# Optimization experiments

Measured on AMD Instinct MI355X. Metric: run time of the kernel, lower is better.

## Reference

```python
import jax, jax.numpy as jnp
import numpy as np

N = 50000; IN_DIM = 128; HID = 128; T = 4; R = 3; E = 500000

def setup_inputs() -> dict:
    key = jax.random.key(0)
    ks = jax.random.split(key, 20)
    def nrm(k, shape, s):
        return jax.random.normal(k, shape, jnp.float32) * s
    s_in = 1.0 / float(np.sqrt(IN_DIM)); s_h = 1.0 / float(np.sqrt(HID))
    return {
        'feat_seq': nrm(ks[0], (T, N, IN_DIM), 1.0),
        'src': jax.random.randint(ks[1], (T, R, E), 0, N, jnp.int32),
        'dst': jax.random.randint(ks[2], (T, R, E), 0, N, jnp.int32),
        'ew': jax.random.uniform(ks[3], (T, R, E), jnp.float32),
        'W_in': nrm(ks[4], (IN_DIM, HID), s_in), 'b_in': jnp.zeros((HID,), jnp.float32),
        'W1': nrm(ks[5], (R, HID, HID), s_h), 'b1': jnp.zeros((R, HID), jnp.float32),
        'W2': nrm(ks[6], (R, HID, HID), s_h), 'b2': jnp.zeros((R, HID), jnp.float32),
        'q1': nrm(ks[7], (HID,), 1.0), 'q2': nrm(ks[8], (HID,), 1.0),
        'ln1_g': jnp.ones((HID,), jnp.float32), 'ln1_b': jnp.zeros((HID,), jnp.float32),
        'ln2_g': jnp.ones((HID,), jnp.float32), 'ln2_b': jnp.zeros((HID,), jnp.float32),
        'gWih': nrm(ks[9], (HID, 3 * HID), s_h), 'gbih': jnp.zeros((3 * HID,), jnp.float32),
        'gWhh': nrm(ks[10], (HID, 3 * HID), s_h), 'gbhh': jnp.zeros((3 * HID,), jnp.float32),
        'temp_q': nrm(ks[11], (HID,), 1.0),
        'tW1': nrm(ks[12], (IN_DIM, HID), s_in), 'tb1': jnp.zeros((HID,), jnp.float32),
        'tW2': nrm(ks[13], (HID, HID), s_h), 'tb2': jnp.zeros((HID,), jnp.float32),
        'cW1': nrm(ks[14], (3 * HID, HID), 1.0 / float(np.sqrt(3 * HID))), 'cb1': jnp.zeros((HID,), jnp.float32),
        'cW2': nrm(ks[15], (HID, 1), s_h), 'cb2': jnp.zeros((1,), jnp.float32),
    }

def _ln(x, g, b):
    m = x.mean(-1, keepdims=True)
    v = ((x - m) ** 2).mean(-1, keepdims=True)
    return (x - m) * jax.lax.rsqrt(v + 1e-5) * g + b

def _rel_attn(stack, q):
    # stack: [R,N,H]; tanh-softmax attention over relations
    score = jnp.einsum('rnh,h->rn', jnp.tanh(stack), q)
    alpha = jax.nn.softmax(score, axis=0)
    return jnp.einsum('rn,rnh->nh', alpha, stack)

def _conv(x, s, d, w, Wr, br):
    # DGL GraphConv norm='right' with edge_weight: mean-by-in-degree weighted SpMM
    msg = w[:, None] * x[s]                                   # [E,H]
    agg = jax.ops.segment_sum(msg, d, num_segments=N)
    deg = jax.ops.segment_sum(jnp.ones_like(w), d, num_segments=N)
    return (agg / jnp.maximum(deg, 1.0)[:, None]) @ Wr + br

def reference(feat_seq, src, dst, ew, W_in, b_in, W1, b1, W2, b2, q1, q2, ln1_g, ln1_b, ln2_g, ln2_b, gWih, gbih, gWhh, gbhh, temp_q, tW1, tb1, tW2, tb2, cW1, cb1, cW2, cb2):
    conv_all = jax.vmap(_conv, in_axes=(None, 0, 0, 0, 0, 0))
    def spatial(x, s, d, w):
        h0 = jax.nn.relu(x @ W_in + b_in)
        h1 = _ln(h0 + jax.nn.relu(_rel_attn(conv_all(h0, s, d, w, W1, b1), q1)), ln1_g, ln1_b)
        h2 = _ln(h1 + jax.nn.relu(_rel_attn(conv_all(h1, s, d, w, W2, b2), q2)), ln2_g, ln2_b)
        return h2
    hs = jnp.stack([spatial(feat_seq[t], src[t], dst[t], ew[t]) for t in range(T)], axis=0)  # [T,N,H]
    def gru_step(h, x):
        gi = x @ gWih + gbih
        gh = h @ gWhh + gbhh
        ir, iz, inn = jnp.split(gi, 3, axis=-1)
        hr, hz, hn = jnp.split(gh, 3, axis=-1)
        r = jax.nn.sigmoid(ir + hr)
        zg = jax.nn.sigmoid(iz + hz)
        n = jnp.tanh(inn + r * hn)
        hnew = (1.0 - zg) * n + zg * h
        return hnew, hnew
    _, outs = jax.lax.scan(gru_step, jnp.zeros((N, HID), feat_seq.dtype), hs)  # [T,N,H]
    out = jnp.transpose(outs, (1, 0, 2))                       # [N,T,H]
    last = out[:, -1, :]
    t_score = jnp.einsum('nth,h->nt', jnp.tanh(out), temp_q)
    t_alpha = jax.nn.softmax(t_score, axis=1)
    attn = jnp.einsum('nt,nth->nh', t_alpha, out)
    tab = jax.nn.relu(jax.nn.relu(feat_seq[-1] @ tW1 + tb1) @ tW2 + tb2)
    z = jnp.concatenate([last, attn, tab], axis=-1)
    return (jax.nn.relu(z @ cW1 + cb1) @ cW2 + cb2)[:, 0]       # [N]
```

## Files before the change

### kernel.cpp

```cpp
#include <hip/hip_runtime.h>
#include <hip/hip_bf16.h>
#include <math.h>

#define NN 50000
#define TT 4
#define RR 3
#define EE 500000
#define RANGE 6400
#define NRANGE 8

typedef __attribute__((ext_vector_type(8))) short bf16x8;
typedef __attribute__((ext_vector_type(4))) float f32x4;

__device__ inline unsigned short f2b(float f)
{
    union { __hip_bfloat16 h; unsigned short u; } cv;
    cv.h = __float2bfloat16(f);
    return cv.u;
}
__device__ inline float b2f(unsigned short u)
{
    union { unsigned int u; float f; } cv;
    cv.u = ((unsigned int)u) << 16;
    return cv.f;
}
__device__ inline bf16x8 pack8(float4 a, float4 b)
{
    bf16x8 r;
    r[0] = (short)f2b(a.x); r[1] = (short)f2b(a.y); r[2] = (short)f2b(a.z); r[3] = (short)f2b(a.w);
    r[4] = (short)f2b(b.x); r[5] = (short)f2b(b.y); r[6] = (short)f2b(b.z); r[7] = (short)f2b(b.w);
    return r;
}


__global__ __launch_bounds__(256)
void diag_kernel(float* __restrict__ out, float v)
{
    int i = blockIdx.x * 256 + threadIdx.x;
    if (i < NN) out[i] = v;
}


__global__ __launch_bounds__(256)
void wswz_kernel(const float* __restrict__ W, unsigned short* __restrict__ dst, int C, int S)
{
    int idx = blockIdx.x * 256 + threadIdx.x;
    int per = 128 * C;
    if (idx >= S * per) return;
    int s = idx / per, rem = idx - s * per;
    int j = rem & 7;
    int lane = (rem >> 3) & 63;
    int blk = rem >> 9;
    int ncg = C >> 4;
    int kc = blk / ncg, cg = blk - kc * ncg;
    int k = kc * 32 + (lane >> 4) * 8 + j;
    int c = cg * 16 + (lane & 15);
    dst[idx] = f2b(W[(size_t)s * 128 * C + (size_t)k * C + c]);
}


__global__ __launch_bounds__(1024)
void count_hist(const int* __restrict__ dst, int* __restrict__ cnt)
{
    __shared__ int hist[RANGE];
    const int g = blockIdx.y;
    const int r0 = blockIdx.x * RANGE;
    for (int i = threadIdx.x; i < RANGE; i += 1024) hist[i] = 0;
    __syncthreads();
    const int4* d4 = (const int4*)(dst + (size_t)g * EE);
    for (int i = threadIdx.x; i < EE / 4; i += 1024) {
        int4 v = d4[i];
        int a0 = v.x - r0; if ((unsigned)a0 < (unsigned)RANGE) atomicAdd(&hist[a0], 1);
        int a1 = v.y - r0; if ((unsigned)a1 < (unsigned)RANGE) atomicAdd(&hist[a1], 1);
        int a2 = v.z - r0; if ((unsigned)a2 < (unsigned)RANGE) atomicAdd(&hist[a2], 1);
        int a3 = v.w - r0; if ((unsigned)a3 < (unsigned)RANGE) atomicAdd(&hist[a3], 1);
    }
    __syncthreads();
    int* c = cnt + (size_t)g * NN;
    for (int i = threadIdx.x; i < RANGE; i += 1024) {
        int n = r0 + i;
        if (n < NN) c[n] = hist[i];
    }
}

__global__ __launch_bounds__(1024)
void scan_kernel(int* __restrict__ cnt, int* __restrict__ rows)
{
    int g = blockIdx.x;
    int tid = threadIdx.x;
    const int CH = (NN + 1023) / 1024;
    int s0 = tid * CH;
    int s1 = s0 + CH; if (s1 > NN) s1 = NN;
    int* c = cnt + (size_t)g * NN;
    int* ro = rows + (size_t)g * (NN + 1);
    int sum = 0;
    for (int i = s0; i < s1; ++i) sum += c[i];
    __shared__ int sd[1024];
    sd[tid] = sum;
    __syncthreads();
    for (int off = 1; off < 1024; off <<= 1) {
        int v = 0;
        if (tid >= off) v = sd[tid - off];
        __syncthreads();
        sd[tid] += v;
        __syncthreads();
    }
    int total = sd[1023];
    int prefix = (tid == 0) ? 0 : sd[tid - 1];
    for (int i = s0; i < s1; ++i) {
        int cv = c[i];
        ro[i] = prefix;
        c[i] = prefix;
        prefix += cv;
    }
    if (tid == 0) ro[NN] = total;
}

__global__ __launch_bounds__(256)
void fill_kernel(const int* __restrict__ src, const int* __restrict__ dst,
                 const float* __restrict__ ew, int* __restrict__ cur,
                 int2* __restrict__ srcw)
{
    int g = blockIdx.y;
    int e = blockIdx.x * 256 + threadIdx.x;
    if (e >= EE) return;
    size_t idx = (size_t)g * EE + e;
    int d = dst[idx];
    int pos = atomicAdd(&cur[(size_t)g * NN + d], 1);
    int2 p;
    p.x = src[idx];
    p.y = __float_as_int(ew[idx]);
    srcw[(size_t)g * EE + pos] = p;
}


__global__ __launch_bounds__(256)
void agg16_kernel(const unsigned short* __restrict__ x16,
                  const int2* __restrict__ srcw,
                  const int* __restrict__ rows,
                  unsigned short* __restrict__ agg16)
{
    int wid = (blockIdx.x * 256 + threadIdx.x) >> 6;
    int lane = threadIdx.x & 63;
    if (wid >= RR * NN) return;
    int r = wid / NN;
    int n = wid - r * NN;
    const int* rs = rows + (size_t)r * (NN + 1);
    int e0 = rs[n], e1 = rs[n + 1];
    const int2* sw = srcw + (size_t)r * EE;
    const int co = lane * 2;
    float ax = 0.f, ay = 0.f;
    for (int e = e0; e < e1; e += 16) {
        int2 p[16];
        unsigned int v[16];
#pragma unroll
        for (int i = 0; i < 16; ++i) {
            int idx = (e + i < e1) ? e + i : e1 - 1;
            p[i] = sw[idx];
        }
#pragma unroll
        for (int i = 0; i < 16; ++i)
            v[i] = *(const unsigned int*)(x16 + (size_t)p[i].x * 128 + co);
#pragma unroll
        for (int i = 0; i < 16; ++i) {
            float w = (e + i < e1) ? __int_as_float(p[i].y) : 0.f;
            ax += w * b2f((unsigned short)(v[i] & 0xffffu));
            ay += w * b2f((unsigned short)(v[i] >> 16));
        }
    }
    float inv = 1.0f / fmaxf((float)(e1 - e0), 1.0f);
    unsigned int o = (unsigned int)f2b(ax * inv) | ((unsigned int)f2b(ay * inv) << 16);
    *(unsigned int*)(agg16 + ((size_t)r * NN + n) * 128 + co) = o;
}


__global__ __launch_bounds__(256)
void mmb(const void* in, int in_bf16, long in_zs, int ldin,
         const unsigned short* __restrict__ Ws, long w_zs,
         const float* __restrict__ bias, long b_zs,
         float* out, long out_zs, int ldout,
         unsigned short* out16, long out16_zs,
         int rows, int act)
{
    const int tid = threadIdx.x;
    const int wv = tid >> 6, l = tid & 63;
    const int z = blockIdx.z;
    const int r0 = blockIdx.x * 64 + wv * 16;
    const int lk = (l >> 4) * 8;
    int rowA = r0 + (l & 15);
    int rowc = rowA < rows ? rowA : rows - 1;

    bf16x8 a[4];
    if (in_bf16) {
        const unsigned short* inb = (const unsigned short*)in + (size_t)z * in_zs
                                    + (size_t)rowc * ldin + lk;
#pragma unroll
        for (int kc = 0; kc < 4; ++kc) {
            uint4 u = *(const uint4*)(inb + kc * 32);
            a[kc] = *(bf16x8*)&u;
        }
    } else {
        const float* inf = (const float*)in + (size_t)z * in_zs
                           + (size_t)rowc * ldin + lk;
#pragma unroll
        for (int kc = 0; kc < 4; ++kc) {
            float4 u0 = *(const float4*)(inf + kc * 32);
            float4 u1 = *(const float4*)(inf + kc * 32 + 4);
            a[kc] = pack8(u0, u1);
        }
    }

    const unsigned short* Wz = Ws + (size_t)z * w_zs;
    const float* bz = bias + (size_t)z * b_zs;
    float* oz = out ? out + (size_t)z * out_zs : (float*)0;
    unsigned short* o16z = out16 ? out16 + (size_t)z * out16_zs : (unsigned short*)0;
    const int colbase = l & 15;
    const int rbase = r0 + (l >> 4) * 4;

#pragma unroll
    for (int cg = 0; cg < 8; ++cg) {
        f32x4 acc = {0.f, 0.f, 0.f, 0.f};
#pragma unroll
        for (int kc = 0; kc < 4; ++kc) {
            uint4 bu = *(const uint4*)(Wz + ((size_t)(kc * 8 + cg) * 64 + l) * 8);
            acc = __builtin_amdgcn_mfma_f32_16x16x32_bf16(a[kc], *(bf16x8*)&bu, acc, 0, 0, 0);
        }
        int col = cg * 16 + colbase;
        float bvv = bz[col];
#pragma unroll
        for (int j = 0; j < 4; ++j) {
            int gr = rbase + j;
            if (gr >= rows) continue;
            float v = acc[j] + bvv;
            if (act) v = fmaxf(v, 0.f);
            if (oz) oz[(size_t)gr * ldout + col] = v;
            if (o16z) o16z[(size_t)gr * 128 + col] = f2b(v);
        }
    }
}


__global__ __launch_bounds__(256)
void grub_all(const float* x, float* h,
              const unsigned short* __restrict__ Wis, const float* __restrict__ bi,
              const unsigned short* __restrict__ Whs, const float* __restrict__ bh,
              float* outs)
{
    const int tid = threadIdx.x;
    const int wv = tid >> 6, l = tid & 63;
    const int r0 = blockIdx.x * 64 + wv * 16;
    const int lk = (l >> 4) * 8;
    int rowA = r0 + (l & 15);
    int rowc = rowA < NN ? rowA : NN - 1;

    bf16x8 ax[4], hx[4];
    {
        const float* bx = x + (size_t)rowc * 128 + lk;
        const float* bhp = h + (size_t)rowc * 128 + lk;
#pragma unroll
        for (int kc = 0; kc < 4; ++kc) {
            ax[kc] = pack8(*(const float4*)(bx + kc * 32), *(const float4*)(bx + kc * 32 + 4));
            hx[kc] = pack8(*(const float4*)(bhp + kc * 32), *(const float4*)(bhp + kc * 32 + 4));
        }
    }
    const int colbase = l & 15;
    const int rbase = r0 + (l >> 4) * 4;

#pragma unroll
    for (int cg = 0; cg < 8; ++cg) {
        f32x4 air = {0.f,0.f,0.f,0.f}, ahr = {0.f,0.f,0.f,0.f};
        f32x4 aiz = {0.f,0.f,0.f,0.f}, ahz = {0.f,0.f,0.f,0.f};
        f32x4 ain = {0.f,0.f,0.f,0.f}, ahn = {0.f,0.f,0.f,0.f};
#pragma unroll
        for (int kc = 0; kc < 4; ++kc) {
            uint4 br = *(const uint4*)(Wis + ((size_t)(kc * 24 + 0 + cg) * 64 + l) * 8);
            uint4 hr = *(const uint4*)(Whs + ((size_t)(kc * 24 + 0 + cg) * 64 + l) * 8);
            uint4 bz = *(const uint4*)(Wis + ((size_t)(kc * 24 + 8 + cg) * 64 + l) * 8);
            uint4 hz = *(const uint4*)(Whs + ((size_t)(kc * 24 + 8 + cg) * 64 + l) * 8);
            uint4 bn = *(const uint4*)(Wis + ((size_t)(kc * 24 + 16 + cg) * 64 + l) * 8);
            uint4 hn = *(const uint4*)(Whs + ((size_t)(kc * 24 + 16 + cg) * 64 + l) * 8);
            air = __builtin_amdgcn_mfma_f32_16x16x32_bf16(ax[kc], *(bf16x8*)&br, air, 0, 0, 0);
            ahr = __builtin_amdgcn_mfma_f32_16x16x32_bf16(hx[kc], *(bf16x8*)&hr, ahr, 0, 0, 0);
            aiz = __builtin_amdgcn_mfma_f32_16x16x32_bf16(ax[kc], *(bf16x8*)&bz, aiz, 0, 0, 0);
            ahz = __builtin_amdgcn_mfma_f32_16x16x32_bf16(hx[kc], *(bf16x8*)&hz, ahz, 0, 0, 0);
            ain = __builtin_amdgcn_mfma_f32_16x16x32_bf16(ax[kc], *(bf16x8*)&bn, ain, 0, 0, 0);
            ahn = __builtin_amdgcn_mfma_f32_16x16x32_bf16(hx[kc], *(bf16x8*)&hn, ahn, 0, 0, 0);
        }
        int col = cg * 16 + colbase;
        float bir = bi[col],       bhr = bh[col];
        float biz = bi[128 + col], bhz = bh[128 + col];
        float bin = bi[256 + col], bhn = bh[256 + col];
#pragma unroll
        for (int j = 0; j < 4; ++j) {
            int gr = rbase + j;
            if (gr >= NN) continue;
            float r_ = 1.f / (1.f + __expf(-(air[j] + bir + ahr[j] + bhr)));
            float z_ = 1.f / (1.f + __expf(-(aiz[j] + biz + ahz[j] + bhz)));
            float n_ = tanhf(ain[j] + bin + r_ * (ahn[j] + bhn));
            float hv = h[(size_t)gr * 128 + col];
            float o = (1.f - z_) * n_ + z_ * hv;
            h[(size_t)gr * 128 + col] = o;
            outs[(size_t)gr * 128 + col] = o;
        }
    }
}


__global__ __launch_bounds__(256)
void cls_mfma(const float* __restrict__ in,
              const unsigned short* __restrict__ Ws,
              const float* __restrict__ b1_,
              const float* __restrict__ w2,
              const float* __restrict__ b2_,
              float* __restrict__ outv, int rows)
{
    const int tid = threadIdx.x;
    const int wv = tid >> 6, l = tid & 63;
    const int r0 = blockIdx.x * 64 + wv * 16;
    const int lk = (l >> 4) * 8;
    int rowA = r0 + (l & 15);
    int rowc = rowA < rows ? rowA : rows - 1;

    bf16x8 a[12];
    {
        const float* inf = in + (size_t)rowc * 384 + lk;
#pragma unroll
        for (int kc = 0; kc < 12; ++kc) {
            float4 u0 = *(const float4*)(inf + kc * 32);
            float4 u1 = *(const float4*)(inf + kc * 32 + 4);
            a[kc] = pack8(u0, u1);
        }
    }
    const int colbase = l & 15;
    const int rbase = r0 + (l >> 4) * 4;
    float part[4] = {0.f, 0.f, 0.f, 0.f};

#pragma unroll
    for (int cg = 0; cg < 8; ++cg) {
        f32x4 acc = {0.f, 0.f, 0.f, 0.f};
#pragma unroll
        for (int kc = 0; kc < 12; ++kc) {
            uint4 bu = *(const uint4*)(Ws + ((size_t)(kc * 8 + cg) * 64 + l) * 8);
            acc = __builtin_amdgcn_mfma_f32_16x16x32_bf16(a[kc], *(bf16x8*)&bu, acc, 0, 0, 0);
        }
        int col = cg * 16 + colbase;
        float b1v = b1_[col];
        float w2v = w2[col];
#pragma unroll
        for (int j = 0; j < 4; ++j)
            part[j] += fmaxf(acc[j] + b1v, 0.f) * w2v;
    }
    const float cb2v = b2_[0];
#pragma unroll
    for (int j = 0; j < 4; ++j) {
#pragma unroll
        for (int m = 1; m < 16; m <<= 1) part[j] += __shfl_xor(part[j], m);
        int gr = rbase + j;
        if ((l & 15) == 0 && gr < rows) outv[gr] = part[j] + cb2v;
    }
}


__device__ inline float wred(float v)
{
#pragma unroll
    for (int m = 32; m; m >>= 1) v += __shfl_xor(v, m);
    return v;
}

__global__ __launch_bounds__(256)
void attnln_kernel(const unsigned short* __restrict__ agg16,
                   const unsigned short* hin16,
                   const float* __restrict__ q,
                   const float* __restrict__ g,
                   const float* __restrict__ b,
                   float* hout,
                   unsigned short* hout16)
{
    int wid = (blockIdx.x * 256 + threadIdx.x) >> 6;
    int lane = threadIdx.x & 63;
    if (wid >= NN) return;
    int n = wid;
    float2 qv = *(const float2*)(q + lane * 2);
    float sx[3], sy[3], sc[3];
#pragma unroll
    for (int r = 0; r < 3; ++r) {
        unsigned int v = *(const unsigned int*)(agg16 + ((size_t)r * NN + n) * 128 + lane * 2);
        sx[r] = b2f((unsigned short)(v & 0xffffu));
        sy[r] = b2f((unsigned short)(v >> 16));
        sc[r] = wred(tanhf(sx[r]) * qv.x + tanhf(sy[r]) * qv.y);
    }
    float mx = fmaxf(sc[0], fmaxf(sc[1], sc[2]));
    float e0 = __expf(sc[0] - mx), e1 = __expf(sc[1] - mx), e2 = __expf(sc[2] - mx);
    float isum = 1.f / (e0 + e1 + e2);
    float axv = (e0 * sx[0] + e1 * sx[1] + e2 * sx[2]) * isum;
    float ayv = (e0 * sy[0] + e1 * sy[1] + e2 * sy[2]) * isum;
    unsigned int hv = *(const unsigned int*)(hin16 + (size_t)n * 128 + lane * 2);
    float ux = b2f((unsigned short)(hv & 0xffffu)) + fmaxf(axv, 0.f);
    float uy = b2f((unsigned short)(hv >> 16)) + fmaxf(ayv, 0.f);
    float mean = wred(ux + uy) * (1.f / 128.f);
    float dx = ux - mean, dy = uy - mean;
    float var = wred(dx * dx + dy * dy) * (1.f / 128.f);
    float rstd = rsqrtf(var + 1e-5f);
    float2 gv = *(const float2*)(g + lane * 2);
    float2 bv = *(const float2*)(b + lane * 2);
    float ox = dx * rstd * gv.x + bv.x;
    float oy = dy * rstd * gv.y + bv.y;
    if (hout) {
        float2 o; o.x = ox; o.y = oy;
        *(float2*)(hout + (size_t)n * 128 + lane * 2) = o;
    }
    if (hout16) {
        unsigned int p = (unsigned int)f2b(ox) | ((unsigned int)f2b(oy) << 16);
        *(unsigned int*)(hout16 + (size_t)n * 128 + lane * 2) = p;
    }
}


__global__ __launch_bounds__(256)
void temporal_kernel(const float* __restrict__ outs,
                     const float* __restrict__ tq,
                     float* __restrict__ zbuf)
{
    int wid = (blockIdx.x * 256 + threadIdx.x) >> 6;
    int lane = threadIdx.x & 63;
    if (wid >= NN) return;
    int n = wid;
    float2 qv = *(const float2*)(tq + lane * 2);
    float2 o[4];
    float sc[4];
#pragma unroll
    for (int t = 0; t < 4; ++t) {
        o[t] = *(const float2*)(outs + ((size_t)t * NN + n) * 128 + lane * 2);
        sc[t] = wred(tanhf(o[t].x) * qv.x + tanhf(o[t].y) * qv.y);
    }
    float mx = fmaxf(fmaxf(sc[0], sc[1]), fmaxf(sc[2], sc[3]));
    float e[4];
    float sum = 0.f;
#pragma unroll
    for (int t = 0; t < 4; ++t) { e[t] = __expf(sc[t] - mx); sum += e[t]; }
    float isum = 1.f / sum;
    float axv = 0.f, ayv = 0.f;
#pragma unroll
    for (int t = 0; t < 4; ++t) { axv += e[t] * o[t].x; ayv += e[t] * o[t].y; }
    axv *= isum; ayv *= isum;
    float* zr = zbuf + (size_t)n * 384;
    *(float2*)(zr + lane * 2) = o[3];
    float2 at; at.x = axv; at.y = ayv;
    *(float2*)(zr + 128 + lane * 2) = at;
}


extern "C" void kernel_launch(void* const* d_in, const int* in_sizes, int n_in,
                              void* d_out, int out_size, void* d_ws, size_t ws_size,
                              hipStream_t stream)
{
    const float* feat = (const float*)d_in[0];
    const int* srcp   = (const int*)d_in[1];
    const int* dstp   = (const int*)d_in[2];
    const float* ewp  = (const float*)d_in[3];
    const float* W_in = (const float*)d_in[4];
    const float* b_in = (const float*)d_in[5];
    const float* W1   = (const float*)d_in[6];
    const float* b1   = (const float*)d_in[7];
    const float* W2   = (const float*)d_in[8];
    const float* b2   = (const float*)d_in[9];
    const float* q1   = (const float*)d_in[10];
    const float* q2   = (const float*)d_in[11];
    const float* ln1g = (const float*)d_in[12];
    const float* ln1b = (const float*)d_in[13];
    const float* ln2g = (const float*)d_in[14];
    const float* ln2b = (const float*)d_in[15];
    const float* gWih = (const float*)d_in[16];
    const float* gbih = (const float*)d_in[17];
    const float* gWhh = (const float*)d_in[18];
    const float* gbhh = (const float*)d_in[19];
    const float* tq   = (const float*)d_in[20];
    const float* tW1  = (const float*)d_in[21];
    const float* tb1  = (const float*)d_in[22];
    const float* tW2  = (const float*)d_in[23];
    const float* tb2  = (const float*)d_in[24];
    const float* cW1  = (const float*)d_in[25];
    const float* cb1  = (const float*)d_in[26];
    const float* cW2  = (const float*)d_in[27];
    const float* cb2  = (const float*)d_in[28];
    float* outv = (float*)d_out;
    (void)in_sizes; (void)n_in; (void)out_size;

    const size_t o_HS    = 0;
    const size_t o_POOL  = 102400000;
    const size_t o_AGG16 = o_POOL;
    const size_t o_H16   = o_POOL + 38400000;
    const size_t o_SRCW  = o_POOL + 51200000;
    const size_t o_ROWS  = o_POOL + 63200000;
    const size_t o_CURS  = o_POOL + 65600128;
    const size_t o_ZB    = o_POOL;
    const size_t o_H     = o_POOL + 76800000;
    const size_t o_WSZ   = o_H + 25600000;
    const size_t NEED    = o_WSZ + 589824;

    if (ws_size < NEED) {
        diag_kernel<<<dim3((NN + 255) / 256), dim3(256), 0, stream>>>(outv, (float)(ws_size >> 20));
        return;
    }

    char* wsb = (char*)d_ws;
    float* HS             = (float*)(wsb + o_HS);
    unsigned short* AGG16 = (unsigned short*)(wsb + o_AGG16);
    unsigned short* H16   = (unsigned short*)(wsb + o_H16);
    int2*  SRCW           = (int2*)(wsb + o_SRCW);
    int*   ROWS           = (int*)(wsb + o_ROWS);
    int*   CURS           = (int*)(wsb + o_CURS);
    float* ZB             = (float*)(wsb + o_ZB);
    float* HST            = (float*)(wsb + o_H);
    unsigned short* TAB16 = (unsigned short*)(wsb + o_H);
    unsigned short* WSZ   = (unsigned short*)(wsb + o_WSZ);

    unsigned short* Wins  = WSZ;
    unsigned short* W1s   = WSZ + 16384;
    unsigned short* W2s   = WSZ + 65536;
    unsigned short* gWihs = WSZ + 114688;
    unsigned short* gWhhs = WSZ + 163840;
    unsigned short* tW1s  = WSZ + 212992;
    unsigned short* tW2s  = WSZ + 229376;
    unsigned short* cW1s  = WSZ + 245760;

    const dim3 blk(256);
    const int G64 = (NN + 63) / 64;
    const dim3 gE((EE + 255) / 256, RR);

    wswz_kernel<<<dim3((1 * 16384 + 255) / 256), blk, 0, stream>>>(W_in, Wins, 128, 1);
    wswz_kernel<<<dim3((3 * 16384 + 255) / 256), blk, 0, stream>>>(W1,   W1s,  128, 3);
    wswz_kernel<<<dim3((3 * 16384 + 255) / 256), blk, 0, stream>>>(W2,   W2s,  128, 3);
    wswz_kernel<<<dim3((1 * 49152 + 255) / 256), blk, 0, stream>>>(gWih, gWihs, 384, 1);
    wswz_kernel<<<dim3((1 * 49152 + 255) / 256), blk, 0, stream>>>(gWhh, gWhhs, 384, 1);
    wswz_kernel<<<dim3((1 * 16384 + 255) / 256), blk, 0, stream>>>(tW1,  tW1s, 128, 1);
    wswz_kernel<<<dim3((1 * 16384 + 255) / 256), blk, 0, stream>>>(tW2,  tW2s, 128, 1);
    wswz_kernel<<<dim3((3 * 16384 + 255) / 256), blk, 0, stream>>>(cW1,  cW1s, 128, 3);

    count_hist<<<dim3(NRANGE, TT * RR), dim3(1024), 0, stream>>>(dstp, CURS);
    scan_kernel<<<dim3(TT * RR), dim3(1024), 0, stream>>>(CURS, ROWS);

    for (int t = 0; t < TT; ++t) {
        const size_t eoff = (size_t)t * RR * EE;
        fill_kernel<<<gE, blk, 0, stream>>>(srcp + eoff, dstp + eoff, ewp + eoff,
                                            CURS + (size_t)t * RR * NN, SRCW);

        mmb<<<dim3(G64, 1, 1), blk, 0, stream>>>(
            (const void*)(feat + (size_t)t * NN * 128), 0, 0, 128,
            Wins, 0, b_in, 0, (float*)0, 0, 0, H16, 0, NN, 1);

        for (int layer = 0; layer < 2; ++layer) {
            const unsigned short* Wls = layer ? W2s : W1s;
            const float* bl = layer ? b2 : b1;
            const float* ql = layer ? q2 : q1;
            const float* lg = layer ? ln2g : ln1g;
            const float* lb = layer ? ln2b : ln1b;
            float* hout = layer ? (HS + (size_t)t * NN * 128) : (float*)0;
            unsigned short* hout16 = layer ? (unsigned short*)0 : H16;

            agg16_kernel<<<dim3((RR * NN) / 4), blk, 0, stream>>>(
                H16, SRCW, ROWS + (size_t)t * RR * (NN + 1), AGG16);
            mmb<<<dim3(G64, 1, RR), blk, 0, stream>>>(
                (const void*)AGG16, 1, (long)NN * 128, 128,
                Wls, 16384, bl, 128, (float*)0, 0, 0, AGG16, (long)NN * 128, NN, 0);
            attnln_kernel<<<dim3(NN / 4), blk, 0, stream>>>(
                AGG16, H16, ql, lg, lb, hout, hout16);
        }
    }

    hipMemsetAsync(HST, 0, (size_t)NN * 128 * 4, stream);
    for (int t = 0; t < TT; ++t) {
        float* xt = HS + (size_t)t * NN * 128;
        grub_all<<<dim3(G64), blk, 0, stream>>>(xt, HST, gWihs, gbih, gWhhs, gbhh, xt);
    }

    temporal_kernel<<<dim3(NN / 4), blk, 0, stream>>>(HS, tq, ZB);

    mmb<<<dim3(G64, 1, 1), blk, 0, stream>>>(
        (const void*)(feat + (size_t)3 * NN * 128), 0, 0, 128,
        tW1s, 0, tb1, 0, (float*)0, 0, 0, TAB16, 0, NN, 1);
    mmb<<<dim3(G64, 1, 1), blk, 0, stream>>>(
        (const void*)TAB16, 1, 0, 128,
        tW2s, 0, tb2, 0, ZB + 256, 0, 384, (unsigned short*)0, 0, NN, 1);

    cls_mfma<<<dim3(G64), blk, 0, stream>>>(ZB, cW1s, cb1, cW2, cb2, outv, NN);
}
```

Before: 2.175 ms.

## Fuse four GRU timesteps into one kernel with hidden state kept on-chip

Replaces the four per-timestep GRU launches and the hidden-state memset with a single kernel that loops over time. The fp32 hidden state stays in registers and a bf16 copy sits in per-wave shared memory as the next step's MFMA operand. This removes the global read and write of the hidden state at every step, plus three launches. The cost is higher register pressure from holding 32 floats of state per lane, which may lower occupancy.

```diff
diff --git a/kernel.cpp b/kernel.cpp
--- a/kernel.cpp
+++ b/kernel.cpp
@@ -241,66 +241,74 @@
 
 
 __global__ __launch_bounds__(256)
-void grub_all(const float* x, float* h,
-              const unsigned short* __restrict__ Wis, const float* __restrict__ bi,
-              const unsigned short* __restrict__ Whs, const float* __restrict__ bh,
-              float* outs)
-{
+void grub4(float* HS,
+           const unsigned short* __restrict__ Wis, const float* __restrict__ bi,
+           const unsigned short* __restrict__ Whs, const float* __restrict__ bh)
+{
+    __shared__ __align__(16) unsigned short hbuf[4][16 * 136];
     const int tid = threadIdx.x;
     const int wv = tid >> 6, l = tid & 63;
     const int r0 = blockIdx.x * 64 + wv * 16;
-    const int lk = (l >> 4) * 8;
-    int rowA = r0 + (l & 15);
-    int rowc = rowA < NN ? rowA : NN - 1;
-
-    bf16x8 ax[4], hx[4];
-    {
-        const float* bx = x + (size_t)rowc * 128 + lk;
-        const float* bhp = h + (size_t)rowc * 128 + lk;
+    const int lo = l & 15, hi = l >> 4;
+    const int lk = hi * 8;
+    const int rowc = (r0 + lo) < NN ? (r0 + lo) : NN - 1;
+    const int rbase = r0 + hi * 4;
+    unsigned short* hb = hbuf[wv];
+
+    for (int i = l; i < 16 * 136; i += 64) hb[i] = 0;
+
+    float hold[8][4];
+#pragma unroll
+    for (int cg = 0; cg < 8; ++cg)
+#pragma unroll
+        for (int j = 0; j < 4; ++j) hold[cg][j] = 0.f;
+
+    for (int t = 0; t < TT; ++t) {
+        float* xt = HS + (size_t)t * NN * 128;
+        bf16x8 ax[4], hx[4];
+        const float* bx = xt + (size_t)rowc * 128 + lk;
 #pragma unroll
         for (int kc = 0; kc < 4; ++kc) {
             ax[kc] = pack8(*(const float4*)(bx + kc * 32), *(const float4*)(bx + kc * 32 + 4));
-            hx[kc] = pack8(*(const float4*)(bhp + kc * 32), *(const float4*)(bhp + kc * 32 + 4));
-        }
-    }
-    const int colbase = l & 15;
-    const int rbase = r0 + (l >> 4) * 4;
-
-#pragma unroll
-    for (int cg = 0; cg < 8; ++cg) {
-        f32x4 air = {0.f,0.f,0.f,0.f}, ahr = {0.f,0.f,0.f,0.f};
-        f32x4 aiz = {0.f,0.f,0.f,0.f}, ahz = {0.f,0.f,0.f,0.f};
-        f32x4 ain = {0.f,0.f,0.f,0.f}, ahn = {0.f,0.f,0.f,0.f};
-#pragma unroll
-        for (int kc = 0; kc < 4; ++kc) {
-            uint4 br = *(const uint4*)(Wis + ((size_t)(kc * 24 + 0 + cg) * 64 + l) * 8);
-            uint4 hr = *(const uint4*)(Whs + ((size_t)(kc * 24 + 0 + cg) * 64 + l) * 8);
-            uint4 bz = *(const uint4*)(Wis + ((size_t)(kc * 24 + 8 + cg) * 64 + l) * 8);
-            uint4 hz = *(const uint4*)(Whs + ((size_t)(kc * 24 + 8 + cg) * 64 + l) * 8);
-            uint4 bn = *(const uint4*)(Wis + ((size_t)(kc * 24 + 16 + cg) * 64 + l) * 8);
-            uint4 hn = *(const uint4*)(Whs + ((size_t)(kc * 24 + 16 + cg) * 64 + l) * 8);
-            air = __builtin_amdgcn_mfma_f32_16x16x32_bf16(ax[kc], *(bf16x8*)&br, air, 0, 0, 0);
-            ahr = __builtin_amdgcn_mfma_f32_16x16x32_bf16(hx[kc], *(bf16x8*)&hr, ahr, 0, 0, 0);
-            aiz = __builtin_amdgcn_mfma_f32_16x16x32_bf16(ax[kc], *(bf16x8*)&bz, aiz, 0, 0, 0);
-            ahz = __builtin_amdgcn_mfma_f32_16x16x32_bf16(hx[kc], *(bf16x8*)&hz, ahz, 0, 0, 0);
-            ain = __builtin_amdgcn_mfma_f32_16x16x32_bf16(ax[kc], *(bf16x8*)&bn, ain, 0, 0, 0);
-            ahn = __builtin_amdgcn_mfma_f32_16x16x32_bf16(hx[kc], *(bf16x8*)&hn, ahn, 0, 0, 0);
-        }
-        int col = cg * 16 + colbase;
-        float bir = bi[col],       bhr = bh[col];
-        float biz = bi[128 + col], bhz = bh[128 + col];
-        float bin = bi[256 + col], bhn = bh[256 + col];
-#pragma unroll
-        for (int j = 0; j < 4; ++j) {
-            int gr = rbase + j;
-            if (gr >= NN) continue;
-            float r_ = 1.f / (1.f + __expf(-(air[j] + bir + ahr[j] + bhr)));
-            float z_ = 1.f / (1.f + __expf(-(aiz[j] + biz + ahz[j] + bhz)));
-            float n_ = tanhf(ain[j] + bin + r_ * (ahn[j] + bhn));
-            float hv = h[(size_t)gr * 128 + col];
-            float o = (1.f - z_) * n_ + z_ * hv;
-            h[(size_t)gr * 128 + col] = o;
-            outs[(size_t)gr * 128 + col] = o;
+            uint4 hu = *(const uint4*)(hb + lo * 136 + kc * 32 + lk);
+            hx[kc] = *(bf16x8*)&hu;
+        }
+
+#pragma unroll
+        for (int cg = 0; cg < 8; ++cg) {
+            f32x4 air = {0.f,0.f,0.f,0.f}, ahr = {0.f,0.f,0.f,0.f};
+            f32x4 aiz = {0.f,0.f,0.f,0.f}, ahz = {0.f,0.f,0.f,0.f};
+            f32x4 ain = {0.f,0.f,0.f,0.f}, ahn = {0.f,0.f,0.f,0.f};
+#pragma unroll
+            for (int kc = 0; kc < 4; ++kc) {
+                uint4 br = *(const uint4*)(Wis + ((size_t)(kc * 24 + 0 + cg) * 64 + l) * 8);
+                uint4 hr = *(const uint4*)(Whs + ((size_t)(kc * 24 + 0 + cg) * 64 + l) * 8);
+                uint4 bz = *(const uint4*)(Wis + ((size_t)(kc * 24 + 8 + cg) * 64 + l) * 8);
+                uint4 hz = *(const uint4*)(Whs + ((size_t)(kc * 24 + 8 + cg) * 64 + l) * 8);
+                uint4 bn = *(const uint4*)(Wis + ((size_t)(kc * 24 + 16 + cg) * 64 + l) * 8);
+                uint4 hn = *(const uint4*)(Whs + ((size_t)(kc * 24 + 16 + cg) * 64 + l) * 8);
+                air = __builtin_amdgcn_mfma_f32_16x16x32_bf16(ax[kc], *(bf16x8*)&br, air, 0, 0, 0);
+                ahr = __builtin_amdgcn_mfma_f32_16x16x32_bf16(hx[kc], *(bf16x8*)&hr, ahr, 0, 0, 0);
+                aiz = __builtin_amdgcn_mfma_f32_16x16x32_bf16(ax[kc], *(bf16x8*)&bz, aiz, 0, 0, 0);
+                ahz = __builtin_amdgcn_mfma_f32_16x16x32_bf16(hx[kc], *(bf16x8*)&hz, ahz, 0, 0, 0);
+                ain = __builtin_amdgcn_mfma_f32_16x16x32_bf16(ax[kc], *(bf16x8*)&bn, ain, 0, 0, 0);
+                ahn = __builtin_amdgcn_mfma_f32_16x16x32_bf16(hx[kc], *(bf16x8*)&hn, ahn, 0, 0, 0);
+            }
+            int col = cg * 16 + lo;
+            float bir = bi[col],       bhr = bh[col];
+            float biz = bi[128 + col], bhz = bh[128 + col];
+            float bin = bi[256 + col], bhn = bh[256 + col];
+#pragma unroll
+            for (int j = 0; j < 4; ++j) {
+                float r_ = 1.f / (1.f + __expf(-(air[j] + bir + ahr[j] + bhr)));
+                float z_ = 1.f / (1.f + __expf(-(aiz[j] + biz + ahz[j] + bhz)));
+                float n_ = tanhf(ain[j] + bin + r_ * (ahn[j] + bhn));
+                float o = (1.f - z_) * n_ + z_ * hold[cg][j];
+                hold[cg][j] = o;
+                int gr = rbase + j;
+                if (gr < NN) xt[(size_t)gr * 128 + col] = o;
+                hb[(hi * 4 + j) * 136 + col] = f2b(o);
+            }
         }
     }
 }
@@ -512,7 +520,6 @@
     int*   ROWS           = (int*)(wsb + o_ROWS);
     int*   CURS           = (int*)(wsb + o_CURS);
     float* ZB             = (float*)(wsb + o_ZB);
-    float* HST            = (float*)(wsb + o_H);
     unsigned short* TAB16 = (unsigned short*)(wsb + o_H);
     unsigned short* WSZ   = (unsigned short*)(wsb + o_WSZ);
 
@@ -569,11 +576,7 @@
         }
     }
 
-    hipMemsetAsync(HST, 0, (size_t)NN * 128 * 4, stream);
-    for (int t = 0; t < TT; ++t) {
-        float* xt = HS + (size_t)t * NN * 128;
-        grub_all<<<dim3(G64), blk, 0, stream>>>(xt, HST, gWihs, gbih, gWhhs, gbhh, xt);
-    }
+    grub4<<<dim3(G64), blk, 0, stream>>>(HS, gWihs, gbih, gWhhs, gbhh);
 
     temporal_kernel<<<dim3(NN / 4), blk, 0, stream>>>(HS, tq, ZB);
 
```

After: 2.594 ms. 19.3% more time.
